# Optimization experiments

Hardware: AMD Instinct MI355X
Metric: run time of the kernel (lower is better)

## Reference

```python
import jax, jax.numpy as jnp
import numpy as np

B, N, NEV, E, D, L = 4, 20000, 100000, 400000, 64, 3

def setup_inputs() -> dict:
    key = jax.random.key(0)
    ks = jax.random.split(key, 12)
    x = jax.random.normal(ks[0], (B, N, 3), dtype=jnp.float32)
    # channel 0 is the susceptible boolean mask (0/1)
    mask0 = (jax.random.uniform(ks[1], (B, N)) < 0.3).astype(jnp.float32)
    x = x.at[..., 0].set(mask0)
    dag_edge_index = jax.random.randint(ks[2], (2, E), 0, NEV, dtype=jnp.int64)
    event_to_node = jax.random.randint(ks[3], (NEV,), 0, N, dtype=jnp.int64)
    event_src_node = jax.random.randint(ks[4], (NEV,), 0, N, dtype=jnp.int64)
    s = 1.0 / np.sqrt(D)
    Wp = jax.random.normal(ks[5], (6, D), dtype=jnp.float32) * (1.0 / np.sqrt(6))
    bp = jnp.zeros((D,), dtype=jnp.float32)
    Ws = jax.random.normal(ks[6], (L, D, D), dtype=jnp.float32) * s
    Wa = jax.random.normal(ks[7], (L, D, D), dtype=jnp.float32) * s
    ba = jnp.zeros((L, D), dtype=jnp.float32)
    Wo = jax.random.normal(ks[8], (D,), dtype=jnp.float32) * s
    bo = jnp.zeros((), dtype=jnp.float32)
    return {"x": x, "Wp": Wp, "bp": bp, "Ws": Ws, "Wa": Wa, "ba": ba,
            "Wo": Wo, "bo": bo, "dag_edge_index": dag_edge_index,
            "event_to_node": event_to_node, "event_src_node": event_src_node}

def reference(x, Wp, bp, Ws, Wa, ba, Wo, bo, dag_edge_index, event_to_node, event_src_node):
    n_events = event_src_node.shape[0]
    # event features: [B, n_events, 6] -> project -> ReLU
    ev_feat = jnp.concatenate([x[:, event_src_node, :], x[:, event_to_node, :]], axis=-1)
    h = jax.nn.relu(ev_feat @ Wp + bp)  # [B, n_events, D]
    # reversed DAG edges: src = dag[1], dst = dag[0]
    src_e, dst_e = dag_edge_index[1], dag_edge_index[0]
    deg = jnp.zeros((n_events,), h.dtype).at[dst_e].add(1.0)
    deg = jnp.maximum(deg, 1.0)[None, :, None]
    for l in range(Ws.shape[0]):
        agg = jnp.zeros_like(h).at[:, dst_e].add(h[:, src_e])  # scatter-add mean agg
        h = jax.nn.relu(h @ Ws[l] + (agg / deg) @ Wa[l] + ba[l])
    # aggregate events back to nodes (mean)
    node_emb = jnp.zeros((x.shape[0], x.shape[1], h.shape[-1]), h.dtype).at[:, event_to_node].add(h)
    count = jnp.zeros((x.shape[1],), h.dtype).at[event_to_node].add(1.0)
    node_emb = node_emb / jnp.maximum(count, 1.0)[None, :, None]
    scores = node_emb @ Wo + bo  # [B, N]
    susceptible = x[..., 0] > 0
    scores = jnp.where(susceptible, -jnp.inf, scores)
    return jax.nn.log_softmax(scores, axis=-1)
```

## Files before the change

kernel.cpp:

```cpp
#include <hip/hip_runtime.h>
#include <hip/hip_bf16.h>
#include <math.h>

constexpr int B   = 4;
constexpr int N   = 20000;
constexpr int NEV = 100000;
constexpr int E   = 400000;
constexpr int D   = 64;
constexpr int L   = 3;
constexpr int XS  = 136;
constexpr int CAP = 32;
constexpr int CHUNK = 625;

typedef short  short8 __attribute__((ext_vector_type(8)));
typedef float  f32x4  __attribute__((ext_vector_type(4)));
typedef float  f32x2  __attribute__((ext_vector_type(2)));


__device__ inline unsigned short f2bu(float f) {
  union { __hip_bfloat16 b; unsigned short s; } u;
  u.b = __float2bfloat16(f);
  return u.s;
}
__device__ inline unsigned packbf(float lo, float hi) {
  return ((unsigned)f2bu(hi) << 16) | (unsigned)f2bu(lo);
}


__global__ void k_zero(float4* __restrict__ p, int n4) {
  int i = blockIdx.x * blockDim.x + threadIdx.x;
  if (i < n4) p[i] = make_float4(0.f, 0.f, 0.f, 0.f);
}

__global__ void k_fill(const int* __restrict__ dag,
                       int* __restrict__ cnt,
                       int* __restrict__ csrc) {
  int i = blockIdx.x * blockDim.x + threadIdx.x;
  if (i >= E) return;
  int dst = dag[i];
  int src = dag[E + i];
  int pos = atomicAdd(&cnt[dst], 1);
  if (pos < CAP) csrc[dst * CAP + pos] = src;
}

__global__ void k_aux(const int* __restrict__ e2n,
                      int* __restrict__ ncount,
                      const float* __restrict__ Ws,
                      const float* __restrict__ Wa,
                      unsigned short* __restrict__ Wt) {
  int bid = blockIdx.x;
  if (bid < 391) {
    int i = bid * 256 + threadIdx.x;
    if (i < NEV) atomicAdd(&ncount[e2n[i]], 1);
  } else {
    int i = (bid - 391) * 256 + threadIdx.x;
    int l = i >> 13;
    int r = i & 8191;
    int n = r >> 7;
    int s = r & 127;
    int sl = (s < 64) ? s : s - 64;
    int c  = (sl & 3) * 16 + (sl >> 2);
    float v = (s < 64) ? Ws[l * 4096 + c * 64 + n]
                       : Wa[l * 4096 + c * 64 + n];
    Wt[l * 8192 + n * 128 + s] = f2bu(v);
  }
}

__global__ __launch_bounds__(256) void k_proj(const float* __restrict__ x,
                                              const float* __restrict__ Wp,
                                              const float* __restrict__ bp,
                                              const int* __restrict__ esrc,
                                              const int* __restrict__ e2n,
                                              unsigned* __restrict__ h) {
  int gid = blockIdx.x * blockDim.x + threadIdx.x;
  int p   = gid & 15;
  int row = gid >> 4;
  int e   = row >> 2;
  int b   = row & 3;
  int sn = esrc[e], tn = e2n[e];
  const float* xs = x + (size_t)(b * N + sn) * 3;
  const float* xt = x + (size_t)(b * N + tn) * 3;
  float xv[6] = {xs[0], xs[1], xs[2], xt[0], xt[1], xt[2]};
  float a[4];
#pragma unroll
  for (int t = 0; t < 4; ++t) {
    int d = p + 16 * t;
    float acc = bp[d];
#pragma unroll
    for (int k = 0; k < 6; ++k) acc += xv[k] * Wp[k * 64 + d];
    a[t] = fmaxf(acc, 0.f);
  }
  int w = __builtin_amdgcn_cvt_pk_fp8_f32(a[0], a[1], 0, false);
  w     = __builtin_amdgcn_cvt_pk_fp8_f32(a[2], a[3], w, true);
  h[row * 16 + p] = (unsigned)w;
}

template <bool LAST>
__global__ __launch_bounds__(256, 6) void k_layer(
    const unsigned short* __restrict__ Wt,
    const float* __restrict__ ba,
    const float* __restrict__ Wo,
    const int* __restrict__ e2n,
    const int* __restrict__ cnt,
    const int* __restrict__ csrc,
    const unsigned char* __restrict__ h_in,
    unsigned char* __restrict__ h_out,
    float* __restrict__ nscore) {
  __shared__ unsigned short sX[64 * XS];
  const int tid  = threadIdx.x;
  const int wv   = tid >> 6, lane = tid & 63;
  const int e0   = blockIdx.x * 16;
  const int r0   = e0 * 4;

  {
    uint4 v = *(const uint4*)(h_in + (size_t)r0 * 64 + tid * 16);
    int row = tid >> 2, ch = tid & 3;
    unsigned vv[4] = {v.x, v.y, v.z, v.w};
    unsigned out[8];
#pragma unroll
    for (int i = 0; i < 4; ++i) {
      f32x2 lo = __builtin_amdgcn_cvt_pk_f32_fp8((int)vv[i], false);
      f32x2 hi = __builtin_amdgcn_cvt_pk_f32_fp8((int)vv[i], true);
      out[2 * i]     = packbf(lo[0], lo[1]);
      out[2 * i + 1] = packbf(hi[0], hi[1]);
    }
    unsigned short* dst = sX + row * XS + ch * 16;
    *(uint4*)dst       = *(uint4*)&out[0];
    *(uint4*)(dst + 8) = *(uint4*)&out[4];
  }

  const int qg = lane >> 4, sub = lane & 15;
  int vidx = csrc[(size_t)(e0 + wv * 4 + qg) * CAP + sub];
  int c_l  = cnt[e0 + wv * 4 + (lane & 3)];

#pragma unroll
  for (int ei = 0; ei < 4; ++ei) {
    int c = __shfl(c_l, ei, 64);
    int cc16 = min(c, 16);
    float a[16];
#pragma unroll
    for (int i = 0; i < 16; ++i) a[i] = 0.f;
    for (int p = 0; p < cc16; p += 4) {
      int j = p + qg;
      if (j < cc16) {
        int s = __shfl(vidx, ei * 16 + j, 64);
        uint4 v = *(const uint4*)(h_in + (size_t)s * 256 + sub * 16);
        unsigned vv[4] = {v.x, v.y, v.z, v.w};
#pragma unroll
        for (int i = 0; i < 4; ++i) {
          f32x2 lo = __builtin_amdgcn_cvt_pk_f32_fp8((int)vv[i], false);
          f32x2 hi = __builtin_amdgcn_cvt_pk_f32_fp8((int)vv[i], true);
          a[4 * i + 0] += lo[0]; a[4 * i + 1] += lo[1];
          a[4 * i + 2] += hi[0]; a[4 * i + 3] += hi[1];
        }
      }
    }
    int cc = min(c, CAP);
    for (int j = 16 + qg; j < cc; j += 4) {
      int s = csrc[(size_t)(e0 + wv * 4 + ei) * CAP + j];
      uint4 v = *(const uint4*)(h_in + (size_t)s * 256 + sub * 16);
      unsigned vv[4] = {v.x, v.y, v.z, v.w};
#pragma unroll
      for (int i = 0; i < 4; ++i) {
        f32x2 lo = __builtin_amdgcn_cvt_pk_f32_fp8((int)vv[i], false);
        f32x2 hi = __builtin_amdgcn_cvt_pk_f32_fp8((int)vv[i], true);
        a[4 * i + 0] += lo[0]; a[4 * i + 1] += lo[1];
        a[4 * i + 2] += hi[0]; a[4 * i + 3] += hi[1];
      }
    }
#pragma unroll
    for (int i = 0; i < 16; ++i) {
      a[i] += __shfl_xor(a[i], 16, 64);
      a[i] += __shfl_xor(a[i], 32, 64);
    }
    if (qg == 0) {
      float inv = 1.f / fmaxf((float)c, 1.f);
      int lrow = (wv * 4 + ei) * 4 + (sub >> 2);
      unsigned out[8];
#pragma unroll
      for (int i = 0; i < 8; ++i)
        out[i] = packbf(a[2 * i] * inv, a[2 * i + 1] * inv);
      unsigned short* dst = sX + lrow * XS + 64 + (sub & 3) * 16;
      *(uint4*)dst       = *(uint4*)&out[0];
      *(uint4*)(dst + 8) = *(uint4*)&out[4];
    }
  }
  __syncthreads();

  const int m = lane & 15, q = lane >> 4;
  f32x4 acc[4];
#pragma unroll
  for (int t = 0; t < 4; ++t) {
    float bv = ba[t * 16 + m];
    acc[t] = (f32x4){bv, bv, bv, bv};
  }
  const unsigned short* xbase = sX + (wv * 16 + m) * XS + q * 8;
  const unsigned short* wbase = Wt + m * 128 + q * 8;
#pragma unroll
  for (int kk = 0; kk < 4; ++kk) {
    short8 av = *(const short8*)(xbase + kk * 32);
#pragma unroll
    for (int t = 0; t < 4; ++t) {
      short8 bv = *(const short8*)(wbase + t * 2048 + kk * 32);
      acc[t] = __builtin_amdgcn_mfma_f32_16x16x32_bf16(av, bv, acc[t], 0, 0, 0);
    }
  }

  if constexpr (!LAST) {
#pragma unroll
    for (int r = 0; r < 4; ++r) {
      int w = __builtin_amdgcn_cvt_pk_fp8_f32(fmaxf(acc[0][r], 0.f),
                                              fmaxf(acc[1][r], 0.f), 0, false);
      w     = __builtin_amdgcn_cvt_pk_fp8_f32(fmaxf(acc[2][r], 0.f),
                                              fmaxf(acc[3][r], 0.f), w, true);
      int grow = r0 + wv * 16 + q * 4 + r;
      ((unsigned*)h_out)[grow * 16 + m] = (unsigned)w;
    }
  } else {
    float w0 = Wo[m], w1 = Wo[16 + m], w2 = Wo[32 + m], w3 = Wo[48 + m];
#pragma unroll
    for (int r = 0; r < 4; ++r) {
      float v = fmaxf(acc[0][r], 0.f) * w0 + fmaxf(acc[1][r], 0.f) * w1
              + fmaxf(acc[2][r], 0.f) * w2 + fmaxf(acc[3][r], 0.f) * w3;
      v += __shfl_xor(v, 1, 64);
      v += __shfl_xor(v, 2, 64);
      v += __shfl_xor(v, 4, 64);
      v += __shfl_xor(v, 8, 64);
      if (m == 0) {
        int grow = r0 + wv * 16 + q * 4 + r;
        int e = grow >> 2, b = grow & 3;
        atomicAdd(&nscore[b * N + e2n[e]], v);
      }
    }
  }
}

__device__ inline float ls_score(const float* nscore, const int* ncount,
                                 const float* x, float bov, int b, int n) {
  return (x[(size_t)(b * N + n) * 3] > 0.f)
             ? -INFINITY
             : nscore[b * N + n] / fmaxf((float)ncount[n], 1.f) + bov;
}

__global__ __launch_bounds__(256) void k_ls1(const float* __restrict__ nscore,
                                             const int* __restrict__ ncount,
                                             const float* __restrict__ x,
                                             const float* __restrict__ bo,
                                             float* __restrict__ pmax,
                                             float* __restrict__ psum) {
  const int b = blockIdx.x >> 5, ch = blockIdx.x & 31;
  const int n0 = ch * CHUNK;
  const int tid = threadIdx.x;
  const float bov = bo[0];
  float s0 = -INFINITY, s1 = -INFINITY, s2 = -INFINITY;
  if (tid < CHUNK)       s0 = ls_score(nscore, ncount, x, bov, b, n0 + tid);
  if (tid + 256 < CHUNK) s1 = ls_score(nscore, ncount, x, bov, b, n0 + tid + 256);
  if (tid + 512 < CHUNK) s2 = ls_score(nscore, ncount, x, bov, b, n0 + tid + 512);
  float m = fmaxf(fmaxf(s0, s1), s2);
  __shared__ float red[4];
#pragma unroll
  for (int o = 32; o; o >>= 1) m = fmaxf(m, __shfl_xor(m, o, 64));
  if ((tid & 63) == 0) red[tid >> 6] = m;
  __syncthreads();
  float pm = fmaxf(fmaxf(red[0], red[1]), fmaxf(red[2], red[3]));
  float pm2 = (pm == -INFINITY) ? 0.f : pm;
  float e = expf(s0 - pm2) + expf(s1 - pm2) + expf(s2 - pm2);
#pragma unroll
  for (int o = 32; o; o >>= 1) e += __shfl_xor(e, o, 64);
  __syncthreads();
  if ((tid & 63) == 0) red[tid >> 6] = e;
  __syncthreads();
  if (tid == 0) {
    pmax[blockIdx.x] = pm;
    psum[blockIdx.x] = red[0] + red[1] + red[2] + red[3];
  }
}

__global__ __launch_bounds__(256) void k_ls3(const float* __restrict__ pmax,
                                             const float* __restrict__ psum,
                                             const float* __restrict__ nscore,
                                             const int* __restrict__ ncount,
                                             const float* __restrict__ x,
                                             const float* __restrict__ bo,
                                             float* __restrict__ out) {
  const int b = blockIdx.x >> 5, ch = blockIdx.x & 31;
  const int n0 = ch * CHUNK;
  const int tid = threadIdx.x;
  const float bov = bo[0];
  __shared__ float sgm, slse;
  if (tid < 64) {
    float pm = (tid < 32) ? pmax[b * 32 + tid] : -INFINITY;
    float ps = (tid < 32) ? psum[b * 32 + tid] : 0.f;
    float gm = pm;
#pragma unroll
    for (int o = 32; o; o >>= 1) gm = fmaxf(gm, __shfl_xor(gm, o, 64));
    float gm2 = (gm == -INFINITY) ? 0.f : gm;
    float c = (pm == -INFINITY) ? 0.f : ps * expf(pm - gm2);
#pragma unroll
    for (int o = 32; o; o >>= 1) c += __shfl_xor(c, o, 64);
    if (tid == 0) { sgm = gm; slse = logf(c); }
  }
  __syncthreads();
  const float gm = sgm, lse = slse;
  for (int i = tid; i < CHUNK; i += 256) {
    int n = n0 + i;
    float s = ls_score(nscore, ncount, x, bov, b, n);
    out[b * N + n] = fmaxf(s - gm - lse, -3.0e38f);
  }
}

extern "C" void kernel_launch(void* const* d_in, const int* in_sizes, int n_in,
                              void* d_out, int out_size, void* d_ws, size_t ws_size,
                              hipStream_t stream) {
  const float* x   = (const float*)d_in[0];
  const float* Wp  = (const float*)d_in[1];
  const float* bp  = (const float*)d_in[2];
  const float* Ws  = (const float*)d_in[3];
  const float* Wa  = (const float*)d_in[4];
  const float* ba  = (const float*)d_in[5];
  const float* Wo  = (const float*)d_in[6];
  const float* bo  = (const float*)d_in[7];
  const int*   dag = (const int*)d_in[8];
  const int*   e2n = (const int*)d_in[9];
  const int*   esr = (const int*)d_in[10];

  int*   ws     = (int*)d_ws;
  int*   cnt    = ws;
  int*   ncount = ws + 100000;
  float* nscore = (float*)(ws + 120000);
  float* pmax   = (float*)(ws + 200000);
  float* psum   = (float*)(ws + 200128);
  int*   csrc   = ws + 200704;
  unsigned short* Wt = (unsigned short*)(ws + 3400704);
  unsigned char* h0 = (unsigned char*)(ws + 3406912);
  unsigned char* h1 = h0 + (size_t)B * NEV * D;
  float* out    = (float*)d_out;

  k_zero<<<(50000 + 255) / 256, 256, 0, stream>>>((float4*)ws, 50000);
  k_fill<<<(E + 255) / 256, 256, 0, stream>>>(dag, cnt, csrc);
  k_aux<<<391 + 96, 256, 0, stream>>>(e2n, ncount, Ws, Wa, Wt);
  k_proj<<<(B * NEV * 16) / 256, 256, 0, stream>>>(x, Wp, bp, esr, e2n,
                                                   (unsigned*)h0);

  k_layer<false><<<NEV / 16, 256, 0, stream>>>(Wt,         ba,       Wo, e2n,
                                               cnt, csrc, h0, h1, nscore);
  k_layer<false><<<NEV / 16, 256, 0, stream>>>(Wt + 8192,  ba + D,   Wo, e2n,
                                               cnt, csrc, h1, h0, nscore);
  k_layer<true><<<NEV / 16, 256, 0, stream>>>(Wt + 16384,  ba + 2*D, Wo, e2n,
                                              cnt, csrc, h0, h1, nscore);

  k_ls1<<<B * 32, 256, 0, stream>>>(nscore, ncount, x, bo, pmax, psum);
  k_ls3<<<B * 32, 256, 0, stream>>>(pmax, psum, nscore, ncount, x, bo, out);
}
```

Measured before the change: 340.7 us.

## Merge prep kernels, move nscore zeroing into proj, and raise layer occupancy

Folds the edge-fill kernel into the aux kernel, so a single prep launch builds the CSR lists, node counts and transposed weights. The zero kernel shrinks because nscore is now cleared inside the projection kernel. The projection kernel has one wavefront per event: 24 lanes load the x values, which are then broadcast with shuffles instead of every lane loading six values. The layer kernel raises its launch-bounds occupancy hint from 6 to 8 and issues the CSR index loads before the LDS staging. The higher occupancy hint may force register spills.

```diff
diff --git a/kernel.cpp b/kernel.cpp
--- a/kernel.cpp
+++ b/kernel.cpp
@@ -32,28 +32,28 @@
   if (i < n4) p[i] = make_float4(0.f, 0.f, 0.f, 0.f);
 }
 
-__global__ void k_fill(const int* __restrict__ dag,
+__global__ void k_prep(const int* __restrict__ dag,
                        int* __restrict__ cnt,
-                       int* __restrict__ csrc) {
-  int i = blockIdx.x * blockDim.x + threadIdx.x;
-  if (i >= E) return;
-  int dst = dag[i];
-  int src = dag[E + i];
-  int pos = atomicAdd(&cnt[dst], 1);
-  if (pos < CAP) csrc[dst * CAP + pos] = src;
-}
-
-__global__ void k_aux(const int* __restrict__ e2n,
-                      int* __restrict__ ncount,
-                      const float* __restrict__ Ws,
-                      const float* __restrict__ Wa,
-                      unsigned short* __restrict__ Wt) {
+                       int* __restrict__ csrc,
+                       const int* __restrict__ e2n,
+                       int* __restrict__ ncount,
+                       const float* __restrict__ Ws,
+                       const float* __restrict__ Wa,
+                       unsigned short* __restrict__ Wt) {
   int bid = blockIdx.x;
-  if (bid < 391) {
+  if (bid < 1563) {
     int i = bid * 256 + threadIdx.x;
+    if (i < E) {
+      int dst = dag[i];
+      int src = dag[E + i];
+      int pos = atomicAdd(&cnt[dst], 1);
+      if (pos < CAP) csrc[dst * CAP + pos] = src;
+    }
+  } else if (bid < 1954) {
+    int i = (bid - 1563) * 256 + threadIdx.x;
     if (i < NEV) atomicAdd(&ncount[e2n[i]], 1);
   } else {
-    int i = (bid - 391) * 256 + threadIdx.x;
+    int i = (bid - 1954) * 256 + threadIdx.x;
     int l = i >> 13;
     int r = i & 8191;
     int n = r >> 7;
@@ -71,16 +71,23 @@
                                               const float* __restrict__ bp,
                                               const int* __restrict__ esrc,
                                               const int* __restrict__ e2n,
-                                              unsigned* __restrict__ h) {
+                                              unsigned* __restrict__ h,
+                                              float* __restrict__ nscore) {
   int gid = blockIdx.x * blockDim.x + threadIdx.x;
-  int p   = gid & 15;
-  int row = gid >> 4;
-  int e   = row >> 2;
-  int b   = row & 3;
+  if (gid < B * N) nscore[gid] = 0.f;
+  const int lane = threadIdx.x & 63;
+  const int e    = gid >> 6;
   int sn = esrc[e], tn = e2n[e];
-  const float* xs = x + (size_t)(b * N + sn) * 3;
-  const float* xt = x + (size_t)(b * N + tn) * 3;
-  float xv[6] = {xs[0], xs[1], xs[2], xt[0], xt[1], xt[2]};
+  float xval = 0.f;
+  if (lane < 24) {
+    int bl = lane / 6, rem = lane % 6;
+    int node = (rem < 3) ? sn : tn;
+    xval = x[(size_t)(bl * N + node) * 3 + (rem < 3 ? rem : rem - 3)];
+  }
+  const int b = lane >> 4, p = lane & 15;
+  float xv[6];
+#pragma unroll
+  for (int k = 0; k < 6; ++k) xv[k] = __shfl(xval, b * 6 + k, 64);
   float a[4];
 #pragma unroll
   for (int t = 0; t < 4; ++t) {
@@ -92,11 +99,11 @@
   }
   int w = __builtin_amdgcn_cvt_pk_fp8_f32(a[0], a[1], 0, false);
   w     = __builtin_amdgcn_cvt_pk_fp8_f32(a[2], a[3], w, true);
-  h[row * 16 + p] = (unsigned)w;
+  h[e * 64 + lane] = (unsigned)w;
 }
 
 template <bool LAST>
-__global__ __launch_bounds__(256, 6) void k_layer(
+__global__ __launch_bounds__(256, 8) void k_layer(
     const unsigned short* __restrict__ Wt,
     const float* __restrict__ ba,
     const float* __restrict__ Wo,
@@ -112,6 +119,10 @@
   const int e0   = blockIdx.x * 16;
   const int r0   = e0 * 4;
 
+  const int qg = lane >> 4, sub = lane & 15;
+  int vidx = csrc[(size_t)(e0 + wv * 4 + qg) * CAP + sub];
+  int c_l  = cnt[e0 + wv * 4 + (lane & 3)];
+
   {
     uint4 v = *(const uint4*)(h_in + (size_t)r0 * 64 + tid * 16);
     int row = tid >> 2, ch = tid & 3;
@@ -128,10 +139,6 @@
     *(uint4*)dst       = *(uint4*)&out[0];
     *(uint4*)(dst + 8) = *(uint4*)&out[4];
   }
-
-  const int qg = lane >> 4, sub = lane & 15;
-  int vidx = csrc[(size_t)(e0 + wv * 4 + qg) * CAP + sub];
-  int c_l  = cnt[e0 + wv * 4 + (lane & 3)];
 
 #pragma unroll
   for (int ei = 0; ei < 4; ++ei) {
@@ -336,11 +343,10 @@
   unsigned char* h1 = h0 + (size_t)B * NEV * D;
   float* out    = (float*)d_out;
 
-  k_zero<<<(50000 + 255) / 256, 256, 0, stream>>>((float4*)ws, 50000);
-  k_fill<<<(E + 255) / 256, 256, 0, stream>>>(dag, cnt, csrc);
-  k_aux<<<391 + 96, 256, 0, stream>>>(e2n, ncount, Ws, Wa, Wt);
+  k_zero<<<(30000 + 255) / 256, 256, 0, stream>>>((float4*)ws, 30000);
+  k_prep<<<2050, 256, 0, stream>>>(dag, cnt, csrc, e2n, ncount, Ws, Wa, Wt);
   k_proj<<<(B * NEV * 16) / 256, 256, 0, stream>>>(x, Wp, bp, esr, e2n,
-                                                   (unsigned*)h0);
+                                                   (unsigned*)h0, nscore);
 
   k_layer<false><<<NEV / 16, 256, 0, stream>>>(Wt,         ba,       Wo, e2n,
                                                cnt, csrc, h0, h1, nscore);
```

New measurement: 336.0 us. Within noise of the previous version (-1.4%).
